# Kernel tuning notes

Measured on AMD Instinct MI355X. Metric: run time of the kernel, lower is better.

The kernel has to match this reference:

```python
import jax, jax.numpy as jnp
import numpy as np

N_NODES = 100000
NEG_SLOPE = 0.2


def _edge_softmax(e, dst, n):
    # softmax over incoming edges of each target node, numerically stable
    m = jax.ops.segment_max(e, dst, num_segments=n)  # [N,H]
    a = jnp.exp(e - m[dst])
    s = jax.ops.segment_sum(a, dst, num_segments=n)  # [N,H]
    return a / (s[dst] + 1e-16)


def _gat_conv(x, src, dst, W, att_src, att_dst, bias):
    # PyG GATConv, concat=False (mean over heads)
    H, F = att_src.shape
    n = x.shape[0]
    h = (x @ W).reshape(n, H, F)              # [N,H,F]
    a_s = jnp.einsum('nhf,hf->nh', h, att_src)  # [N,H]
    a_d = jnp.einsum('nhf,hf->nh', h, att_dst)
    e = a_s[src] + a_d[dst]                   # [E,H]
    e = jax.nn.leaky_relu(e, NEG_SLOPE)
    alpha = _edge_softmax(e, dst, n)          # [E,H]
    msg = h[src] * alpha[:, :, None]          # [E,H,F] (largest intermediate)
    out = jax.ops.segment_sum(msg, dst, num_segments=n)  # [N,H,F]
    return out.mean(axis=1) + bias            # [N,F]


def setup_inputs() -> dict:
    key = jax.random.key(0)
    ks = jax.random.split(key, 10)
    in_f, h_f, out_f, heads = 128, 32, 16, 8
    E = 1600000
    x = jax.random.normal(ks[0], (N_NODES, in_f), dtype=jnp.float32)
    edge_index = jax.random.randint(ks[1], (2, E), 0, N_NODES, dtype=jnp.int32)
    s1 = 1.0 / np.sqrt(in_f)
    s2 = 1.0 / np.sqrt(h_f)
    return {
        'x': x,
        'edge_index': edge_index,
        'W1': jax.random.normal(ks[2], (in_f, heads * h_f), dtype=jnp.float32) * s1,
        'att_src1': jax.random.normal(ks[3], (heads, h_f), dtype=jnp.float32) * s2,
        'att_dst1': jax.random.normal(ks[4], (heads, h_f), dtype=jnp.float32) * s2,
        'b1': jnp.zeros((h_f,), dtype=jnp.float32),
        'W2': jax.random.normal(ks[5], (h_f, heads * out_f), dtype=jnp.float32) * s2,
        'att_src2': jax.random.normal(ks[6], (heads, out_f), dtype=jnp.float32) * 0.25,
        'att_dst2': jax.random.normal(ks[7], (heads, out_f), dtype=jnp.float32) * 0.25,
        'b2': jnp.zeros((out_f,), dtype=jnp.float32),
    }


def reference(x, edge_index, W1, att_src1, att_dst1, b1, W2, att_src2, att_dst2, b2):
    src, dst = edge_index[0], edge_index[1]
    # eval mode: dropout(p=0.6) is identity
    h = _gat_conv(x, src, dst, W1, att_src1, att_dst1, b1)
    h = jax.nn.relu(h)
    out = _gat_conv(h, src, dst, W2, att_src2, att_dst2, b2)
    return out
```

## Files before the change

### kernel.cpp

```cpp
#include <hip/hip_runtime.h>
#include <hip/hip_fp16.h>


__device__ __forceinline__ float lrelu_exp(float v) {
    v = v > 0.f ? v : 0.2f * v;
    return __expf(v);
}

__global__ __launch_bounds__(256) void k_zero(float* __restrict__ p, int n) {
    int i = blockIdx.x * 256 + threadIdx.x;
    const int stride = gridDim.x * 256;
    for (; i < n; i += stride) p[i] = 0.f;
}

__global__ __launch_bounds__(256) void k_zero_int(int* __restrict__ p, int n) {
    int i = blockIdx.x * 256 + threadIdx.x;
    const int stride = gridDim.x * 256;
    for (; i < n; i += stride) p[i] = 0;
}

__global__ __launch_bounds__(256) void k_bhist(const int* __restrict__ ei,
                                               int* __restrict__ gcnt,
                                               int E, int nblk, int nbkt) {
    __shared__ int cnt[256];
    const int t = threadIdx.x;
    cnt[t] = 0;
    __syncthreads();
    const int base = blockIdx.x * 4096;
#pragma unroll
    for (int i = 0; i < 16; ++i) {
        const int e = base + i * 256 + t;
        if (e < E) atomicAdd(&cnt[ei[E + e] >> 9], 1);
    }
    __syncthreads();
    if (t < nbkt) gcnt[t * nblk + blockIdx.x] = cnt[t];
}

__global__ __launch_bounds__(256) void k_scan_block2(int* __restrict__ g,
                                                     int* __restrict__ bsum, int L) {
    __shared__ int s[256];
    const int t = threadIdx.x;
    const int i = blockIdx.x * 256 + t;
    const int v = (i < L) ? g[i] : 0;
    s[t] = v;
    __syncthreads();
    for (int off = 1; off < 256; off <<= 1) {
        const int tv = (t >= off) ? s[t - off] : 0;
        __syncthreads();
        s[t] += tv;
        __syncthreads();
    }
    if (i < L) g[i] = s[t] - v;
    if (t == 255) bsum[blockIdx.x] = s[255];
}

__global__ __launch_bounds__(1024) void k_scan_sums(int* __restrict__ bsum, int NB) {
    __shared__ int s[1024];
    const int t = threadIdx.x;
    const int v = (t < NB) ? bsum[t] : 0;
    s[t] = v;
    __syncthreads();
    for (int off = 1; off < 1024; off <<= 1) {
        const int tv = (t >= off) ? s[t - off] : 0;
        __syncthreads();
        s[t] += tv;
        __syncthreads();
    }
    if (t < NB) bsum[t] = s[t] - v;
}

__global__ __launch_bounds__(256) void k_scan_add2(int* __restrict__ g,
                                                   const int* __restrict__ bsum, int L) {
    const int i = blockIdx.x * 256 + threadIdx.x;
    if (i < L) g[i] += bsum[blockIdx.x];
}

__global__ __launch_bounds__(256) void k_bucket_scatter(const int* __restrict__ ei,
                                                        const int* __restrict__ gbase,
                                                        int2* __restrict__ buf2,
                                                        int E, int nblk, int nbkt) {
    __shared__ int cnt[256];
    __shared__ int sbase[256];
    const int t = threadIdx.x;
    cnt[t] = 0;
    if (t < nbkt) sbase[t] = gbase[t * nblk + blockIdx.x];
    __syncthreads();
    const int base = blockIdx.x * 4096;
#pragma unroll
    for (int i = 0; i < 16; ++i) {
        const int e = base + i * 256 + t;
        if (e < E) {
            const int src = ei[e];
            const int dst = ei[E + e];
            const int b = dst >> 9;
            const int r = atomicAdd(&cnt[b], 1);
            buf2[sbase[b] + r] = make_int2(src, dst);
        }
    }
}

__global__ __launch_bounds__(256) void k_bucket_csr(const int2* __restrict__ buf2,
                                                    const int* __restrict__ gbase,
                                                    int* __restrict__ rowptr,
                                                    int* __restrict__ esrc,
                                                    int* __restrict__ sdst,
                                                    int N, int E, int nblk, int nbkt) {
    __shared__ int hist[512], curs[512], ps[256];
    __shared__ int sh_base, sh_end;
    const int t = threadIdx.x;
    const int b = blockIdx.x;
    const int node0 = b << 9;
    if (t == 0) {
        sh_base = gbase[b * nblk];
        sh_end  = (b + 1 < nbkt) ? gbase[(b + 1) * nblk] : E;
        if (b == 0) rowptr[N] = E;
    }
    hist[t] = 0;
    hist[t + 256] = 0;
    __syncthreads();
    const int eb = sh_base, ee = sh_end;
    for (int e = eb + t; e < ee; e += 256)
        atomicAdd(&hist[buf2[e].y - node0], 1);
    __syncthreads();
    const int p0 = hist[2 * t], p1 = hist[2 * t + 1];
    const int pr = p0 + p1;
    ps[t] = pr;
    __syncthreads();
    for (int off = 1; off < 256; off <<= 1) {
        const int v = (t >= off) ? ps[t - off] : 0;
        __syncthreads();
        ps[t] += v;
        __syncthreads();
    }
    const int e0 = ps[t] - pr;
    curs[2 * t]     = e0;
    curs[2 * t + 1] = e0 + p0;
    const int nn = min(512, N - node0);
    if (2 * t < nn)     rowptr[node0 + 2 * t]     = eb + e0;
    if (2 * t + 1 < nn) rowptr[node0 + 2 * t + 1] = eb + e0 + p0;
    __syncthreads();
    for (int e = eb + t; e < ee; e += 256) {
        const int2 r = buf2[e];
        const int rk = atomicAdd(&curs[r.y - node0], 1);
        esrc[eb + rk] = r.x;
        sdst[eb + rk] = r.y;
    }
}

__global__ __launch_bounds__(256) void k_hist(const int* __restrict__ ei,
                                              int* __restrict__ deg, int E) {
    const int e = blockIdx.x * 256 + threadIdx.x;
    if (e < E) atomicAdd(&deg[ei[E + e]], 1);
}

__global__ __launch_bounds__(256) void k_scan_block(const int* __restrict__ deg,
                                                    int* __restrict__ rowptr,
                                                    int* __restrict__ bsum, int N) {
    __shared__ int s[256];
    const int t = threadIdx.x;
    const int i = blockIdx.x * 256 + t;
    const int v = (i < N) ? deg[i] : 0;
    s[t] = v;
    __syncthreads();
    for (int off = 1; off < 256; off <<= 1) {
        const int tv = (t >= off) ? s[t - off] : 0;
        __syncthreads();
        s[t] += tv;
        __syncthreads();
    }
    if (i < N) rowptr[i] = s[t] - v;
    if (t == 255) bsum[blockIdx.x] = s[255];
}

__global__ __launch_bounds__(256) void k_scan_add(int* __restrict__ rowptr,
                                                  const int* __restrict__ bsum,
                                                  int* __restrict__ cursor, int N, int E) {
    const int i = blockIdx.x * 256 + threadIdx.x;
    if (i < N) {
        const int r = rowptr[i] + bsum[blockIdx.x];
        rowptr[i] = r;
        cursor[i] = r;
    }
    if (i == 0) rowptr[N] = E;
}

__global__ __launch_bounds__(256) void k_scatter(const int* __restrict__ ei,
                                                 int* __restrict__ cursor,
                                                 int* __restrict__ esrc, int E) {
    const int e = blockIdx.x * 256 + threadIdx.x;
    if (e >= E) return;
    const int src = ei[e];
    const int dst = ei[E + e];
    const int pos = atomicAdd(&cursor[dst], 1);
    esrc[pos] = src;
}

template <int IN, int C, int F>
__global__ __launch_bounds__(256) void k_gemm_big(const float* __restrict__ x,
                                                  const float* __restrict__ W,
                                                  __half* __restrict__ h, int N) {
    constexpr int CJ = C / 32;
    constexpr int KC = 16;
    __shared__ float xs[32 * IN];
    __shared__ float wlds[KC * (C + 4)];
    const int t  = threadIdx.x;
    const int n0 = blockIdx.x * 32;

    const float4* src4 = (const float4*)(x + (size_t)n0 * IN);
    float4* xs4 = (float4*)xs;
    constexpr int NV = 32 * IN / 4;
    for (int idx = t; idx < NV; idx += 256) {
        const int row = idx / (IN / 4);
        xs4[idx] = (n0 + row < N) ? src4[idx] : make_float4(0.f, 0.f, 0.f, 0.f);
    }

    const int tc = t & 31;
    const int tr = t >> 5;
    float acc[4][CJ];
#pragma unroll
    for (int i = 0; i < 4; ++i)
#pragma unroll
        for (int j = 0; j < CJ; ++j) acc[i][j] = 0.f;

#pragma unroll 1
    for (int kc = 0; kc < IN; kc += KC) {
        __syncthreads();
        for (int idx = t; idx < KC * C; idx += 256) {
            const int k = idx / C, c = idx % C;
            wlds[k * (C + 4) + c] = W[(size_t)(kc + k) * C + c];
        }
        __syncthreads();
#pragma unroll 1
        for (int q = 0; q < KC / 4; ++q) {
            float4 xv[4];
#pragma unroll
            for (int i = 0; i < 4; ++i)
                xv[i] = *(const float4*)&xs[(tr * 4 + i) * IN + kc + q * 4];
#pragma unroll
            for (int kk = 0; kk < 4; ++kk) {
                float wv[CJ];
#pragma unroll
                for (int j = 0; j < CJ; ++j)
                    wv[j] = wlds[(q * 4 + kk) * (C + 4) + tc + j * 32];
#pragma unroll
                for (int i = 0; i < 4; ++i) {
                    const float xvv = ((const float*)&xv[i])[kk];
#pragma unroll
                    for (int j = 0; j < CJ; ++j)
                        acc[i][j] = fmaf(xvv, wv[j], acc[i][j]);
                }
            }
        }
    }

    if constexpr (C == 256 && F == 32) {
#pragma unroll
        for (int i = 0; i < 4; ++i) {
            const int r = n0 + tr * 4 + i;
            if (r < N) {
                __half tmp[8];
#pragma unroll
                for (int j = 0; j < 8; ++j) tmp[j] = __float2half(acc[i][j]);
                *(float4*)(h + (size_t)r * 256 + tc * 8) = *(const float4*)tmp;
            }
        }
    } else {
#pragma unroll
        for (int i = 0; i < 4; ++i) {
            const int r = n0 + tr * 4 + i;
            if (r < N) {
#pragma unroll
                for (int j = 0; j < CJ; ++j) {
                    const int c = tc + j * 32;
                    h[(size_t)r * C + (c % F) * 8 + (c / F)] = __float2half(acc[i][j]);
                }
            }
        }
    }
}

template <int F, int HG>
__global__ __launch_bounds__(256) void k_dots_h(const __half* __restrict__ h,
                                                const float* __restrict__ atts,
                                                const float* __restrict__ attd,
                                                float* __restrict__ as_,
                                                float* __restrict__ ad_, int N, int hb) {
    const int i = blockIdx.x * 256 + threadIdx.x;
    if (i >= N * HG) return;
    const int n  = i / HG;
    const int hl = i % HG;
    const int hg = hb + hl;
    const __half* hp = h + (size_t)n * (F * HG) + hl;
    const float* sv = atts + hg * F;
    const float* dv = attd + hg * F;
    float s = 0.f, d = 0.f;
#pragma unroll
    for (int f = 0; f < F; ++f) {
        const float v = __half2float(hp[f * HG]);
        s = fmaf(v, sv[f], s);
        d = fmaf(v, dv[f], d);
    }
    as_[(size_t)n * 8 + hg] = s;
    ad_[(size_t)n * 8 + hg] = d;
}

__global__ __launch_bounds__(256) void k_alpha_csr(const int* __restrict__ esrc,
                                                   const int* __restrict__ sdst,
                                                   const float* __restrict__ as_,
                                                   const float* __restrict__ ad_,
                                                   __half* __restrict__ exbuf, int E) {
    const int p = blockIdx.x * 256 + threadIdx.x;
    if (p >= E) return;
    const int src = esrc[p];
    const int dst = sdst[p];
    const float4 s0 = *(const float4*)(as_ + (size_t)src * 8);
    const float4 s1 = *(const float4*)(as_ + (size_t)src * 8 + 4);
    const float4 d0 = *(const float4*)(ad_ + (size_t)dst * 8);
    const float4 d1 = *(const float4*)(ad_ + (size_t)dst * 8 + 4);
    __half tmp[8];
    tmp[0] = __float2half(lrelu_exp(s0.x + d0.x));
    tmp[1] = __float2half(lrelu_exp(s0.y + d0.y));
    tmp[2] = __float2half(lrelu_exp(s0.z + d0.z));
    tmp[3] = __float2half(lrelu_exp(s0.w + d0.w));
    tmp[4] = __float2half(lrelu_exp(s1.x + d1.x));
    tmp[5] = __float2half(lrelu_exp(s1.y + d1.y));
    tmp[6] = __float2half(lrelu_exp(s1.z + d1.z));
    tmp[7] = __float2half(lrelu_exp(s1.w + d1.w));
    *(float4*)(exbuf + (size_t)p * 8) = *(const float4*)tmp;
}

__global__ __launch_bounds__(256) void k_rinv(const int* __restrict__ rowptr,
                                              const __half* __restrict__ exbuf,
                                              float* __restrict__ rinv, int N) {
    const int i = blockIdx.x * 256 + threadIdx.x;
    if (i >= N * 8) return;
    const int n  = i >> 3;
    const int hh = i & 7;
    const int r0 = rowptr[n], r1 = rowptr[n + 1];
    float den = 0.f;
    for (int e = r0; e < r1; ++e)
        den += __half2float(exbuf[(size_t)e * 8 + hh]);
    rinv[i] = 1.f / (den + 1e-16f);
}

template <int F, int MODE>
__global__ __launch_bounds__(256) void k_agg_ex3(const int* __restrict__ rowptr,
                                                 const int* __restrict__ esrc,
                                                 const __half* __restrict__ exbuf,
                                                 const float* __restrict__ rinv,
                                                 const __half* __restrict__ h,
                                                 const float* __restrict__ bias,
                                                 float* __restrict__ outp, int N) {
    constexpr int NPB = 256 / F;
    const int n = blockIdx.x * NPB + threadIdx.x / F;
    const int f = threadIdx.x % F;
    if (n >= N) return;
    const int r0 = rowptr[n], r1 = rowptr[n + 1];

    float accA[8], accB[8];
#pragma unroll
    for (int k = 0; k < 8; ++k) { accA[k] = 0.f; accB[k] = 0.f; }

    int e = r0;
    for (; e + 2 <= r1; e += 2) {
        const int s0 = esrc[e];
        const int s1 = esrc[e + 1];
        const float4 ex0 = *(const float4*)(exbuf + (size_t)e * 8);
        const float4 ex1 = *(const float4*)(exbuf + (size_t)(e + 1) * 8);
        const float4 h0  = *(const float4*)(h + (size_t)s0 * (F * 8) + f * 8);
        const float4 h1  = *(const float4*)(h + (size_t)s1 * (F * 8) + f * 8);
        const __half2* e20 = (const __half2*)&ex0;
        const __half2* h20 = (const __half2*)&h0;
        const __half2* e21 = (const __half2*)&ex1;
        const __half2* h21 = (const __half2*)&h1;
#pragma unroll
        for (int k = 0; k < 4; ++k) {
            const float2 ef0 = __half22float2(e20[k]);
            const float2 hf0 = __half22float2(h20[k]);
            accA[2 * k]     = fmaf(ef0.x, hf0.x, accA[2 * k]);
            accA[2 * k + 1] = fmaf(ef0.y, hf0.y, accA[2 * k + 1]);
            const float2 ef1 = __half22float2(e21[k]);
            const float2 hf1 = __half22float2(h21[k]);
            accB[2 * k]     = fmaf(ef1.x, hf1.x, accB[2 * k]);
            accB[2 * k + 1] = fmaf(ef1.y, hf1.y, accB[2 * k + 1]);
        }
    }
    if (e < r1) {
        const int s0 = esrc[e];
        const float4 ex0 = *(const float4*)(exbuf + (size_t)e * 8);
        const float4 h0  = *(const float4*)(h + (size_t)s0 * (F * 8) + f * 8);
        const __half2* e20 = (const __half2*)&ex0;
        const __half2* h20 = (const __half2*)&h0;
#pragma unroll
        for (int k = 0; k < 4; ++k) {
            const float2 ef0 = __half22float2(e20[k]);
            const float2 hf0 = __half22float2(h20[k]);
            accA[2 * k]     = fmaf(ef0.x, hf0.x, accA[2 * k]);
            accA[2 * k + 1] = fmaf(ef0.y, hf0.y, accA[2 * k + 1]);
        }
    }
    const float* rv = rinv + (size_t)n * 8;
    float s = 0.f;
#pragma unroll
    for (int k = 0; k < 8; ++k) s += (accA[k] + accB[k]) * rv[k];
    float v = 0.125f * s + bias[f];
    if constexpr (MODE == 1) v = v > 0.f ? v : 0.f;
    outp[(size_t)n * F + f] = v;
}

template <int IN, int C, int OW, int F>
__global__ __launch_bounds__(256) void k_gemm_h(const float* __restrict__ x,
                                                const float* __restrict__ W,
                                                __half* __restrict__ h, int N, int c0) {
    constexpr int HG = C / F;
    __shared__ float xs[32 * IN];
    const int t  = threadIdx.x;
    const int n0 = blockIdx.x * 32;
    const float4* src4 = (const float4*)(x + (size_t)n0 * IN);
    float4* xs4 = (float4*)xs;
    constexpr int NV = 32 * IN / 4;
    for (int idx = t; idx < NV; idx += 256) {
        const int row = idx / (IN / 4);
        xs4[idx] = (n0 + row < N) ? src4[idx] : make_float4(0.f, 0.f, 0.f, 0.f);
    }
    __syncthreads();
    const int idx = t % C;
    const int r0  = t / C;
    constexpr int RSTEP = 256 / C;
    constexpr int RPT   = 32 / RSTEP;
    const int f  = idx / HG;
    const int hd = idx % HG;
    float acc[RPT];
#pragma unroll
    for (int i = 0; i < RPT; ++i) acc[i] = 0.f;
    const float* Wc = W + c0 + hd * F + f;
#pragma unroll 1
    for (int k = 0; k < IN; k += 4) {
        const float w0 = Wc[(k + 0) * OW];
        const float w1 = Wc[(k + 1) * OW];
        const float w2 = Wc[(k + 2) * OW];
        const float w3 = Wc[(k + 3) * OW];
#pragma unroll
        for (int i = 0; i < RPT; ++i) {
            const int r = r0 + i * RSTEP;
            const float4 xv = *(const float4*)&xs[r * IN + k];
            acc[i] = fmaf(xv.x, w0, fmaf(xv.y, w1, fmaf(xv.z, w2, fmaf(xv.w, w3, acc[i]))));
        }
    }
#pragma unroll
    for (int i = 0; i < RPT; ++i) {
        const int r = r0 + i * RSTEP;
        if (n0 + r < N) h[(size_t)(n0 + r) * C + idx] = __float2half(acc[i]);
    }
}

template <int HG>
__global__ __launch_bounds__(256) void k_denom(const int* __restrict__ rowptr,
                                               const int* __restrict__ esrc,
                                               const float* __restrict__ as_,
                                               const float* __restrict__ ad_,
                                               float* __restrict__ rinv, int N, int hb) {
    const int i = blockIdx.x * 256 + threadIdx.x;
    if (i >= N * HG) return;
    const int n  = i / HG;
    const int hl = i % HG;
    const float ad = ad_[(size_t)n * 8 + hb + hl];
    const int r0 = rowptr[n];
    const int r1 = rowptr[n + 1];
    float s = 0.f;
    for (int e = r0; e < r1; ++e)
        s += lrelu_exp(as_[(size_t)esrc[e] * 8 + hb + hl] + ad);
    rinv[(size_t)n * 8 + hb + hl] = 1.f / (s + 1e-16f);
}

template <int F, int HG>
__global__ __launch_bounds__(256) void k_csr_agg_hg(const int* __restrict__ rowptr,
                                                    const int* __restrict__ esrc,
                                                    const float* __restrict__ as_,
                                                    const float* __restrict__ ad_,
                                                    const float* __restrict__ rinv,
                                                    const __half* __restrict__ h,
                                                    float* __restrict__ outp,
                                                    int N, int hb) {
    constexpr int NPB = 256 / F;
    const int n = blockIdx.x * NPB + threadIdx.x / F;
    const int f = threadIdx.x % F;
    if (n >= N) return;
    const int r0 = rowptr[n];
    const int r1 = rowptr[n + 1];
    float ad[HG], rv[HG];
#pragma unroll
    for (int k = 0; k < HG; ++k) {
        ad[k] = ad_[(size_t)n * 8 + hb + k];
        rv[k] = rinv[(size_t)n * 8 + hb + k];
    }
    float a0 = 0.f;
    for (int e = r0; e < r1; ++e) {
        const int src = esrc[e];
        const float* sp = as_ + (size_t)src * 8 + hb;
        const __half* hp = h + (size_t)src * (F * HG) + f * HG;
#pragma unroll
        for (int k = 0; k < HG; ++k) {
            const float al = lrelu_exp(sp[k] + ad[k]) * rv[k];
            a0 = fmaf(al, __half2float(hp[k]), a0);
        }
    }
    outp[(size_t)n * F + f] += 0.125f * a0;
}

__global__ __launch_bounds__(256) void k_relu_bias(float* __restrict__ a,
                                                   const float* __restrict__ b, int total) {
    const int i = blockIdx.x * 256 + threadIdx.x;
    if (i < total) {
        const float v = a[i] + b[i & 31];
        a[i] = v > 0.f ? v : 0.f;
    }
}

__global__ __launch_bounds__(256) void k_bias_inplace(float* __restrict__ a,
                                                      const float* __restrict__ b, int total) {
    const int i = blockIdx.x * 256 + threadIdx.x;
    if (i < total) a[i] += b[i & 15];
}

static void run_full(const float* x, const int* ei,
                     const float* W1, const float* as1, const float* ad1, const float* b1,
                     const float* W2, const float* as2, const float* ad2, const float* b2,
                     float* out, int N, int E, char* ws, hipStream_t stream) {
    auto align256 = [](size_t b) { return (b + 255) & ~(size_t)255; };
    size_t off = 0;
    auto alloc = [&](size_t bytes) { char* p = ws + off; off += align256(bytes); return p; };

    const int NBLKC = (E + 4095) / 4096;
    const int nbkt  = (N + 511) >> 9;
    const int L     = nbkt * NBLKC;

    __half* hbuf  = (__half*)alloc((size_t)N * 256 * 2);
    __half* exbuf = (__half*)alloc((size_t)E * 8 * 2);
    float* a_s    = (float*)alloc((size_t)N * 8 * 4);
    float* a_d    = (float*)alloc((size_t)N * 8 * 4);
    float* rinv   = (float*)alloc((size_t)N * 8 * 4);
    size_t acc_bytes = (size_t)N * 32 * 4;
    size_t buf2_bytes = (size_t)E * 8;
    float* acc1   = (float*)alloc(acc_bytes > buf2_bytes ? acc_bytes : buf2_bytes);
    int2* buf2    = (int2*)acc1;
    int* rowptr   = (int*)alloc((size_t)(N + 1) * 4);
    int* esrc     = (int*)alloc((size_t)E * 4);
    int* sdst     = (int*)alloc((size_t)E * 4);
    int* gcnt     = (int*)alloc((size_t)L * 4);
    int* bsum2    = (int*)alloc(1024 * 4);

    const int NBs = (L + 255) / 256;
    k_bhist<<<NBLKC, 256, 0, stream>>>(ei, gcnt, E, NBLKC, nbkt);
    k_scan_block2<<<NBs, 256, 0, stream>>>(gcnt, bsum2, L);
    k_scan_sums<<<1, 1024, 0, stream>>>(bsum2, NBs);
    k_scan_add2<<<NBs, 256, 0, stream>>>(gcnt, bsum2, L);
    k_bucket_scatter<<<NBLKC, 256, 0, stream>>>(ei, gcnt, buf2, E, NBLKC, nbkt);
    k_bucket_csr<<<nbkt, 256, 0, stream>>>(buf2, gcnt, rowptr, esrc, sdst, N, E, NBLKC, nbkt);

    const int NBg = (N + 31) / 32;
    const int nbp = (N * 8 + 255) / 256;
    const int NBe = (E + 255) / 256;
    k_gemm_big<128, 256, 32><<<NBg, 256, 0, stream>>>(x, W1, hbuf, N);
    k_dots_h<32, 8><<<nbp, 256, 0, stream>>>(hbuf, as1, ad1, a_s, a_d, N, 0);
    k_alpha_csr<<<NBe, 256, 0, stream>>>(esrc, sdst, a_s, a_d, exbuf, E);
    k_rinv<<<nbp, 256, 0, stream>>>(rowptr, exbuf, rinv, N);
    k_agg_ex3<32, 1><<<(N + 7) / 8, 256, 0, stream>>>(rowptr, esrc, exbuf, rinv, hbuf, b1, acc1, N);
    k_gemm_big<32, 128, 16><<<NBg, 256, 0, stream>>>(acc1, W2, hbuf, N);
    k_dots_h<16, 8><<<nbp, 256, 0, stream>>>(hbuf, as2, ad2, a_s, a_d, N, 0);
    k_alpha_csr<<<NBe, 256, 0, stream>>>(esrc, sdst, a_s, a_d, exbuf, E);
    k_rinv<<<nbp, 256, 0, stream>>>(rowptr, exbuf, rinv, N);
    k_agg_ex3<16, 2><<<(N + 15) / 16, 256, 0, stream>>>(rowptr, esrc, exbuf, rinv, hbuf, b2, out, N);
}

static void run_fallback4(const float* x, const int* ei,
                          const float* W1, const float* as1, const float* ad1, const float* b1,
                          const float* W2, const float* as2, const float* ad2, const float* b2,
                          float* out, int N, int E, char* ws, hipStream_t stream) {
    constexpr int HG = 4;
    auto align256 = [](size_t b) { return (b + 255) & ~(size_t)255; };
    size_t off = 0;
    auto alloc = [&](size_t bytes) { char* p = ws + off; off += align256(bytes); return p; };

    __half* hbuf = (__half*)alloc((size_t)N * HG * 32 * 2);
    float* a_s   = (float*)alloc((size_t)N * 8 * 4);
    float* a_d   = (float*)alloc((size_t)N * 8 * 4);
    float* rinv  = (float*)alloc((size_t)N * 8 * 4);
    float* acc1  = (float*)alloc((size_t)N * 32 * 4);
    int* rowptr  = (int*)alloc((size_t)(N + 1) * 4);
    int* cursor  = (int*)alloc((size_t)N * 4);
    int* deg     = (int*)alloc((size_t)N * 4);
    int* bsum    = (int*)alloc(1024 * 4);
    int* esrc    = (int*)alloc((size_t)E * 4);

    const int NBn = (N + 255) / 256;
    const int NBe = (E + 255) / 256;
    k_zero_int<<<512, 256, 0, stream>>>(deg, N);
    k_hist<<<NBe, 256, 0, stream>>>(ei, deg, E);
    k_scan_block<<<NBn, 256, 0, stream>>>(deg, rowptr, bsum, N);
    k_scan_sums<<<1, 1024, 0, stream>>>(bsum, NBn);
    k_scan_add<<<NBn, 256, 0, stream>>>(rowptr, bsum, cursor, N, E);
    k_scatter<<<NBe, 256, 0, stream>>>(ei, cursor, esrc, E);

    k_zero<<<512, 256, 0, stream>>>(acc1, N * 32);
    k_zero<<<512, 256, 0, stream>>>(out, N * 16);

    const int nbp = (N * HG + 255) / 256;
    for (int g = 0; g < 2; ++g) {
        k_gemm_h<128, 128, 256, 32><<<NBn * 8, 256, 0, stream>>>(x, W1, hbuf, N, g * 128);
        k_dots_h<32, HG><<<nbp, 256, 0, stream>>>(hbuf, as1, ad1, a_s, a_d, N, g * HG);
        k_denom<HG><<<nbp, 256, 0, stream>>>(rowptr, esrc, a_s, a_d, rinv, N, g * HG);
        k_csr_agg_hg<32, HG><<<(N + 7) / 8, 256, 0, stream>>>(rowptr, esrc, a_s, a_d, rinv,
                                                              hbuf, acc1, N, g * HG);
    }
    k_relu_bias<<<(N * 32 + 255) / 256, 256, 0, stream>>>(acc1, b1, N * 32);

    for (int g = 0; g < 2; ++g) {
        k_gemm_h<32, 64, 128, 16><<<NBn * 8, 256, 0, stream>>>(acc1, W2, hbuf, N, g * 64);
        k_dots_h<16, HG><<<nbp, 256, 0, stream>>>(hbuf, as2, ad2, a_s, a_d, N, g * HG);
        k_denom<HG><<<nbp, 256, 0, stream>>>(rowptr, esrc, a_s, a_d, rinv, N, g * HG);
        k_csr_agg_hg<16, HG><<<(N + 15) / 16, 256, 0, stream>>>(rowptr, esrc, a_s, a_d, rinv,
                                                                hbuf, out, N, g * HG);
    }
    k_bias_inplace<<<(N * 16 + 255) / 256, 256, 0, stream>>>(out, b2, N * 16);
}

extern "C" void kernel_launch(void* const* d_in, const int* in_sizes, int n_in,
                              void* d_out, int out_size, void* d_ws, size_t ws_size,
                              hipStream_t stream) {
    const float* x   = (const float*)d_in[0];
    const int*   ei  = (const int*)d_in[1];
    const float* W1  = (const float*)d_in[2];
    const float* as1 = (const float*)d_in[3];
    const float* ad1 = (const float*)d_in[4];
    const float* b1  = (const float*)d_in[5];
    const float* W2  = (const float*)d_in[6];
    const float* as2 = (const float*)d_in[7];
    const float* ad2 = (const float*)d_in[8];
    const float* b2  = (const float*)d_in[9];
    float* out = (float*)d_out;

    const int N = in_sizes[0] / 128;
    const int E = in_sizes[1] / 2;

    const int NBLKC = (E + 4095) / 4096;
    const int nbkt  = (N + 511) >> 9;
    const int L     = nbkt * NBLKC;
    const size_t acc_or_buf2 = ((size_t)N * 32 * 4 > (size_t)E * 8) ? (size_t)N * 32 * 4
                                                                    : (size_t)E * 8;
    const size_t need_full = (size_t)2 * N * 256 + (size_t)2 * E * 8 +
                             (size_t)4 * N * 24 + acc_or_buf2 +
                             (size_t)4 * (N + 1) + (size_t)8 * E +
                             (size_t)4 * L + 4096 + 20 * 256;
    char* ws = (char*)d_ws;
    if (ws_size >= need_full && nbkt <= 256 && (L + 255) / 256 <= 1024) {
        run_full(x, ei, W1, as1, ad1, b1, W2, as2, ad2, b2, out, N, E, ws, stream);
    } else {
        run_fallback4(x, ei, W1, as1, ad1, b1, W2, as2, ad2, b2, out, N, E, ws, stream);
    }
}
```

Measured before the change: 468.9 us.

## Use MFMA fp16 matrix cores for first-layer GEMM with pre-transposed half weights

Replaces the scalar-FMA first-layer GEMM (128->256) with a kernel that converts x to fp16 in LDS, stages a pre-transposed fp16 copy of W1, and uses 16x16x32 f16 MFMA instructions. The output is restaged through LDS so it can be written to global memory as vector stores in the head-interleaved layout. An extra small kernel converts and transposes W1 on every call. The change lowers input precision to fp16 for the GEMM and removes the now-unused specialized store path from the old kernel.

```diff
diff --git a/kernel.cpp b/kernel.cpp
--- a/kernel.cpp
+++ b/kernel.cpp
@@ -1,6 +1,9 @@
 #include <hip/hip_runtime.h>
 #include <hip/hip_fp16.h>
 
+
+typedef _Float16 f16x8 __attribute__((ext_vector_type(8)));
+typedef float f32x4 __attribute__((ext_vector_type(4)));
 
 __device__ __forceinline__ float lrelu_exp(float v) {
     v = v > 0.f ? v : 0.2f * v;
@@ -195,6 +198,91 @@
     esrc[pos] = src;
 }
 
+__global__ __launch_bounds__(256) void k_prep_w(const float* __restrict__ W,
+                                                __half* __restrict__ wt, int K, int C) {
+    const int i = blockIdx.x * 256 + threadIdx.x;
+    if (i >= K * C) return;
+    const int c = i % C;
+    const int k = i / C;
+    wt[(size_t)c * K + k] = __float2half(W[(size_t)k * C + c]);
+}
+
+__global__ __launch_bounds__(256) void k_gemm_mfma1(const float* __restrict__ x,
+                                                    const __half* __restrict__ wt,
+                                                    __half* __restrict__ h, int N) {
+    constexpr int PADX = 136;
+    constexpr int WTS  = 40;
+    constexpr int HSS  = 264;
+    __shared__ __align__(16) __half xs16[32 * PADX];
+    __shared__ __align__(16) __half wbuf[256 * WTS];
+    __half* hs = wbuf;
+
+    const int t    = threadIdx.x;
+    const int n0   = blockIdx.x * 32;
+    const int lane = t & 63;
+    const int w    = t >> 6;
+    const int rg   = w >> 1;
+    const int ct0  = (w & 1) * 8;
+    const int lr   = lane & 15;
+    const int g    = lane >> 4;
+
+    for (int p = 0; p < 4; ++p) {
+        const int idx = p * 256 + t;
+        const int row = idx >> 5;
+        const int q   = idx & 31;
+        float4 v = make_float4(0.f, 0.f, 0.f, 0.f);
+        if (n0 + row < N) v = *(const float4*)(x + (size_t)(n0 + row) * 128 + q * 4);
+        __half2* dst = (__half2*)(xs16 + row * PADX + q * 4);
+        dst[0] = __floats2half2_rn(v.x, v.y);
+        dst[1] = __floats2half2_rn(v.z, v.w);
+    }
+
+    f32x4 acc[8];
+#pragma unroll
+    for (int j = 0; j < 8; ++j) acc[j] = (f32x4){0.f, 0.f, 0.f, 0.f};
+
+#pragma unroll 1
+    for (int kc = 0; kc < 128; kc += 32) {
+        __syncthreads();
+        for (int p = 0; p < 4; ++p) {
+            const int idx  = p * 256 + t;
+            const int c    = idx >> 2;
+            const int part = idx & 3;
+            const f16x8 vv = *(const f16x8*)(wt + (size_t)c * 128 + kc + part * 8);
+            *(f16x8*)(wbuf + c * WTS + part * 8) = vv;
+        }
+        __syncthreads();
+        const f16x8 a = *(const f16x8*)(xs16 + (rg * 16 + lr) * PADX + kc + g * 8);
+#pragma unroll
+        for (int j = 0; j < 8; ++j) {
+            const f16x8 b = *(const f16x8*)(wbuf + ((ct0 + j) * 16 + lr) * WTS + g * 8);
+            acc[j] = __builtin_amdgcn_mfma_f32_16x16x32_f16(a, b, acc[j], 0, 0, 0);
+        }
+    }
+
+    __syncthreads();
+#pragma unroll
+    for (int j = 0; j < 8; ++j) {
+        const int c   = (ct0 + j) * 16 + lr;
+        const int idx = (c & 31) * 8 + (c >> 5);
+#pragma unroll
+        for (int r = 0; r < 4; ++r) {
+            const int row = rg * 16 + g * 4 + r;
+            hs[row * HSS + idx] = __float2half(acc[j][r]);
+        }
+    }
+    __syncthreads();
+    for (int p = 0; p < 4; ++p) {
+        const int idx = p * 256 + t;
+        const int row = idx >> 5;
+        const int q   = idx & 31;
+        if (n0 + row < N) {
+            const f16x8 vv = *(const f16x8*)(hs + row * HSS + q * 8);
+            *(f16x8*)(h + (size_t)(n0 + row) * 256 + q * 8) = vv;
+        }
+    }
+}
+
 template <int IN, int C, int F>
 __global__ __launch_bounds__(256) void k_gemm_big(const float* __restrict__ x,
                                                   const float* __restrict__ W,
@@ -253,27 +341,14 @@
         }
     }
 
-    if constexpr (C == 256 && F == 32) {
-#pragma unroll
-        for (int i = 0; i < 4; ++i) {
-            const int r = n0 + tr * 4 + i;
-            if (r < N) {
-                __half tmp[8];
-#pragma unroll
-                for (int j = 0; j < 8; ++j) tmp[j] = __float2half(acc[i][j]);
-                *(float4*)(h + (size_t)r * 256 + tc * 8) = *(const float4*)tmp;
-            }
-        }
-    } else {
-#pragma unroll
-        for (int i = 0; i < 4; ++i) {
-            const int r = n0 + tr * 4 + i;
-            if (r < N) {
-#pragma unroll
-                for (int j = 0; j < CJ; ++j) {
-                    const int c = tc + j * 32;
-                    h[(size_t)r * C + (c % F) * 8 + (c / F)] = __float2half(acc[i][j]);
-                }
+#pragma unroll
+    for (int i = 0; i < 4; ++i) {
+        const int r = n0 + tr * 4 + i;
+        if (r < N) {
+#pragma unroll
+            for (int j = 0; j < CJ; ++j) {
+                const int c = tc + j * 32;
+                h[(size_t)r * C + (c % F) * 8 + (c / F)] = __float2half(acc[i][j]);
             }
         }
     }
@@ -537,6 +612,7 @@
 
     __half* hbuf  = (__half*)alloc((size_t)N * 256 * 2);
     __half* exbuf = (__half*)alloc((size_t)E * 8 * 2);
+    __half* wt16  = (__half*)alloc((size_t)256 * 128 * 2);
     float* a_s    = (float*)alloc((size_t)N * 8 * 4);
     float* a_d    = (float*)alloc((size_t)N * 8 * 4);
     float* rinv   = (float*)alloc((size_t)N * 8 * 4);
@@ -561,7 +637,8 @@
     const int NBg = (N + 31) / 32;
     const int nbp = (N * 8 + 255) / 256;
     const int NBe = (E + 255) / 256;
-    k_gemm_big<128, 256, 32><<<NBg, 256, 0, stream>>>(x, W1, hbuf, N);
+    k_prep_w<<<(128 * 256 + 255) / 256, 256, 0, stream>>>(W1, wt16, 128, 256);
+    k_gemm_mfma1<<<NBg, 256, 0, stream>>>(x, wt16, hbuf, N);
     k_dots_h<32, 8><<<nbp, 256, 0, stream>>>(hbuf, as1, ad1, a_s, a_d, N, 0);
     k_alpha_csr<<<NBe, 256, 0, stream>>>(esrc, sdst, a_s, a_d, exbuf, E);
     k_rinv<<<nbp, 256, 0, stream>>>(rowptr, exbuf, rinv, N);
@@ -649,9 +726,10 @@
     const size_t acc_or_buf2 = ((size_t)N * 32 * 4 > (size_t)E * 8) ? (size_t)N * 32 * 4
                                                                     : (size_t)E * 8;
     const size_t need_full = (size_t)2 * N * 256 + (size_t)2 * E * 8 +
+                             (size_t)2 * 256 * 128 +
                              (size_t)4 * N * 24 + acc_or_buf2 +
                              (size_t)4 * (N + 1) + (size_t)8 * E +
-                             (size_t)4 * L + 4096 + 20 * 256;
+                             (size_t)4 * L + 4096 + 24 * 256;
     char* ws = (char*)d_ws;
     if (ws_size >= need_full && nbkt <= 256 && (L + 255) / 256 <= 1024) {
         run_full(x, ei, W1, as1, ad1, b1, W2, as2, ad2, b2, out, N, E, ws, stream);
```

Result: faster. 394.4 us (-15.9%).
